# Optimization experiments

Measured on AMD Instinct MI355X. Metric: run time of the kernel, lower is better.

The kernel has to match this reference:

```python
import math
import jax, jax.numpy as jnp
import numpy as np

N, DIN, DOUT = 32768, 1024, 1024
C = 1.0            # ball curvature c (k = -c)
MIN_NORM = 1e-15
EPS_PROJ = 4e-3    # geoopt float32 boundary eps


def _safe_norm(x):
    # sqrt of clipped sum-of-squares: finite value and finite grad at 0
    return jnp.sqrt(jnp.clip(jnp.sum(x * x, axis=-1, keepdims=True), MIN_NORM))


def _artanh(u):
    return jnp.arctanh(jnp.clip(u, -1.0 + 1e-5, 1.0 - 1e-5))


def _project(x, c):
    norm = _safe_norm(x)
    maxnorm = (1.0 - EPS_PROJ) / jnp.sqrt(c)
    return jnp.where(norm > maxnorm, x / norm * maxnorm, x)


def _mobius_matvec(W, x, c):
    sqc = jnp.sqrt(c)
    x_norm = _safe_norm(x)                       # [N,1]
    mx = x @ W.T                                 # [N,DOUT]
    mx_norm = _safe_norm(mx)                     # [N,1]
    res = jnp.tanh(mx_norm / x_norm * _artanh(sqc * x_norm)) * mx / (mx_norm * sqc)
    zero = jnp.all(mx == 0, axis=-1, keepdims=True)
    return jnp.where(zero, jnp.zeros((), x.dtype), res)


def _expmap0(u, c):
    sqc = jnp.sqrt(c)
    u_norm = _safe_norm(u)
    return jnp.tanh(sqc * u_norm) * u / (sqc * u_norm)


def _mobius_add(x, y, c):
    x2 = jnp.sum(x * x, axis=-1, keepdims=True)
    y2 = jnp.sum(y * y, axis=-1, keepdims=True)
    xy = jnp.sum(x * y, axis=-1, keepdims=True)
    num = (1.0 + 2.0 * c * xy + c * y2) * x + (1.0 - c * x2) * y
    denom = 1.0 + 2.0 * c * xy + c * c * x2 * y2
    return num / jnp.clip(denom, MIN_NORM)


def setup_inputs() -> dict:
    key = jax.random.key(0)
    kx, kw, kb = jax.random.split(key, 3)
    x = jax.random.normal(kx, (N, DIN), jnp.float32)
    # place points strictly inside the unit Poincare ball
    x = x / (jnp.linalg.norm(x, axis=-1, keepdims=True) + 1.0) * 0.7
    limit = math.sqrt(2.0) * math.sqrt(6.0 / (DIN + DOUT))  # xavier_uniform gain=sqrt(2)
    weight = jax.random.uniform(kw, (DOUT, DIN), jnp.float32, -limit, limit)
    bias = 0.01 * jax.random.normal(kb, (DOUT,), jnp.float32)
    return {"x": x, "weight": weight, "bias": bias}


def reference(x, weight, bias) -> jnp.ndarray:
    c = jnp.float32(C)
    res = _mobius_matvec(weight, x, c)           # dropout=0 / eval: weight used as-is
    res = _project(res, c)
    hyp_bias = _project(_expmap0(bias[None, :], c), c)
    res = _project(_mobius_add(res, hyp_bias, c), c)
    return res
```

## Files before the change

kernel.cpp:

```cpp
#include <hip/hip_runtime.h>
#include <hip/hip_bf16.h>
#include <cmath>

#define NROWS 32768
#define DIN   1024
#define DOUT  1024
#define BM    64
#define BK    32
#define NKT   (DIN / BK)
#define MAXNORM 0.996f
#define XPAD  40

typedef __attribute__((ext_vector_type(8))) __bf16 bf16x8;
typedef __attribute__((ext_vector_type(4))) float  f32x4;
typedef __attribute__((ext_vector_type(2))) float  f32x2;
typedef __attribute__((ext_vector_type(4))) unsigned u32x4;

__device__ __forceinline__ unsigned pack2bf(float a, float b) {
    union { unsigned u; __bf16 h[2]; } p;
    p.h[0] = (__bf16)a; p.h[1] = (__bf16)b;
    return p.u;
}

__global__ void conv_w_kernel(const float* __restrict__ Wf, __bf16* __restrict__ Wb) {
    int c  = blockIdx.x * blockDim.x + threadIdx.x;
    int l  = c & 63;
    int j  = (c >> 6) & 63;
    int kt = c >> 12;
    int n  = j * 16 + (l & 15);
    int k0 = kt * 32 + (l >> 4) * 8;
    const float* src = Wf + (size_t)n * DIN + k0;
    f32x4 v0 = __builtin_nontemporal_load((const f32x4*)src);
    f32x4 v1 = __builtin_nontemporal_load((const f32x4*)(src + 4));
    u32x4 o;
    o.x = pack2bf(v0[0], v0[1]); o.y = pack2bf(v0[2], v0[3]);
    o.z = pack2bf(v1[0], v1[1]); o.w = pack2bf(v1[2], v1[3]);
    *(u32x4*)((char*)Wb + (size_t)c * 16) = o;
}

__global__ __launch_bounds__(1024) void hyp_kernel_reg(
    const float* __restrict__ X,
    const __bf16* __restrict__ Wb,
    const float* __restrict__ bias,
    float* __restrict__ out)
{
    __shared__ __align__(16) __bf16 Xt[4][BM * XPAD];
    __shared__ float hbs[DOUT];
    __shared__ float xsqs[BM];
    __shared__ float fco[BM][2];
    __shared__ float bred[16];

    const int tid  = threadIdx.x;
    const int lane = tid & 63;
    const int wid  = tid >> 6;
    const int l15  = lane & 15;
    const int l4   = lane >> 4;
    const int row0 = blockIdx.x * BM;

    const int xr = tid >> 4;
    const int xk = (tid & 15) * 2;
    const float* xp = X + (size_t)(row0 + xr) * DIN + xk;
    float xsq = 0.f;

    const __bf16* wp = Wb + ((size_t)(wid * 4) * 64 + lane) * 8;

    f32x4 acc[4][4];
    #pragma unroll
    for (int m = 0; m < 4; m++)
        #pragma unroll
        for (int n = 0; n < 4; n++)
            acc[m][n] = (f32x4){0.f, 0.f, 0.f, 0.f};

    f32x2 x0 = __builtin_nontemporal_load((const f32x2*)xp);
    f32x2 x1 = __builtin_nontemporal_load((const f32x2*)(xp + BK));
    bf16x8 bfr[4];
    #pragma unroll
    for (int i = 0; i < 4; i++) bfr[i] = *(const bf16x8*)(wp + i * 512);

    float bv = bias[tid];
    float bs = bv * bv;
    #pragma unroll
    for (int m = 1; m < 64; m <<= 1) bs += __shfl_xor(bs, m);
    if (lane == 0) bred[wid] = bs;
    __syncthreads();
    float tot = 0.f;
    #pragma unroll
    for (int i = 0; i < 16; i++) tot += bred[i];
    const float bnorm = sqrtf(fmaxf(tot, 1e-15f));
    const float bth   = tanhf(bnorm);
    float sc0 = bth / bnorm;
    float hn  = bth;
    if (hn > MAXNORM) { sc0 *= MAXNORM / hn; hn = MAXNORM; }
    hbs[tid] = sc0 * bv;
    const float y2c = hn * hn;

    xsq += x0[0] * x0[0] + x0[1] * x0[1];
    *(unsigned*)((char*)(&Xt[0][0]) + xr * (XPAD * 2) + xk * 2) = pack2bf(x0[0], x0[1]);
    x0 = x1;
    x1 = __builtin_nontemporal_load((const f32x2*)(xp + 2 * BK));

    auto step = [&](int s, int rb, int wb) {
        asm volatile("s_waitcnt lgkmcnt(0)" ::: "memory");
        __builtin_amdgcn_s_barrier();
        __builtin_amdgcn_sched_barrier(0);

        const char* xb = (const char*)(&Xt[rb][0]);
        bf16x8 a[4];
        #pragma unroll
        for (int m = 0; m < 4; m++)
            a[m] = *(const bf16x8*)(xb + ((m << 4) + l15) * (XPAD * 2) + (l4 << 4));

        if (s + 1 < NKT) {
            xsq += x0[0] * x0[0] + x0[1] * x0[1];
            *(unsigned*)((char*)(&Xt[wb][0]) + xr * (XPAD * 2) + xk * 2) = pack2bf(x0[0], x0[1]);
        }
        x0 = x1;
        int sf = s + 3 < NKT ? s + 3 : NKT - 1;
        x1 = __builtin_nontemporal_load((const f32x2*)(xp + (size_t)sf * BK));

        __builtin_amdgcn_s_setprio(1);
        #pragma unroll
        for (int n = 0; n < 4; n++)
            #pragma unroll
            for (int m = 0; m < 4; m++)
                acc[m][n] = __builtin_amdgcn_mfma_f32_16x16x32_bf16(a[m], bfr[n], acc[m][n], 0, 0, 0);
        __builtin_amdgcn_s_setprio(0);

        int sb = s + 1 < NKT ? s + 1 : NKT - 1;
        const __bf16* wkp = wp + (size_t)sb * 32768;
        #pragma unroll
        for (int i = 0; i < 4; i++) bfr[i] = *(const bf16x8*)(wkp + i * 512);
    };

    for (int s = 0; s < NKT; s += 4) {
        step(s + 0, 0, 1);
        step(s + 1, 1, 2);
        step(s + 2, 2, 3);
        step(s + 3, 3, 0);
    }

    __syncthreads();

    float* redq = (float*)(&Xt[0][0]);
    float* redd = redq + BM * 16;

    float xs = xsq;
    #pragma unroll
    for (int m = 1; m < 16; m <<= 1) xs += __shfl_xor(xs, m);
    if (l15 == 0) xsqs[xr] = xs;

    float hv[4];
    #pragma unroll
    for (int n = 0; n < 4; n++) hv[n] = hbs[(wid << 6) + (n << 4) + l15];

    #pragma unroll
    for (int m = 0; m < 4; m++) {
        #pragma unroll
        for (int r = 0; r < 4; r++) {
            float s = 0.f, d = 0.f;
            #pragma unroll
            for (int n = 0; n < 4; n++) {
                float v = acc[m][n][r];
                s += v * v;
                d += v * hv[n];
            }
            #pragma unroll
            for (int mm = 1; mm < 16; mm <<= 1) {
                s += __shfl_xor(s, mm);
                d += __shfl_xor(d, mm);
            }
            if (l15 == 0) {
                int rl = (m << 4) + (l4 << 2) + r;
                redq[rl * 16 + wid] = s;
                redd[rl * 16 + wid] = d;
            }
        }
    }
    __syncthreads();

    if (tid < BM) {
        int r = tid;
        float sq = 0.f, dt = 0.f;
        #pragma unroll
        for (int w = 0; w < 16; w++) { sq += redq[r * 16 + w]; dt += redd[r * 16 + w]; }
        float sx     = xsqs[r];
        float xnorm  = sqrtf(fmaxf(sx, 1e-15f));
        float mxnorm = sqrtf(fmaxf(sq, 1e-15f));
        float u  = fminf(xnorm, 1.f - 1e-5f);
        float tv = tanhf(mxnorm / xnorm * atanhf(u));
        float rn = fminf(tv, MAXNORM);
        float s  = rn / mxnorm;
        float xy = s * dt;
        float x2 = rn * rn;
        float Am = 1.f + 2.f * xy + y2c;
        float Bm = 1.f - x2;
        float Dm = fmaxf(1.f + 2.f * xy + x2 * y2c, 1e-15f);
        float g1 = Am * s / Dm;
        float g2 = Bm / Dm;
        float osq   = g1 * g1 * sq + 2.f * g1 * g2 * dt + g2 * g2 * y2c;
        float onorm = sqrtf(fmaxf(osq, 1e-15f));
        float psc   = onorm > MAXNORM ? MAXNORM / onorm : 1.f;
        fco[r][0] = g1 * psc;
        fco[r][1] = g2 * psc;
    }
    __syncthreads();

    #pragma unroll
    for (int m = 0; m < 4; m++) {
        #pragma unroll
        for (int r = 0; r < 4; r++) {
            int rl = (m << 4) + (l4 << 2) + r;
            float F1 = fco[rl][0], F2 = fco[rl][1];
            float* orow = out + (size_t)(row0 + rl) * DOUT + (wid << 6);
            #pragma unroll
            for (int n = 0; n < 4; n++)
                orow[(n << 4) + l15] = F1 * acc[m][n][r] + F2 * hv[n];
        }
    }
}

__global__ __launch_bounds__(512, 2) void hyp_kernel_basic(
    const float* __restrict__ X,
    const float* __restrict__ Wf,
    const float* __restrict__ bias,
    float* __restrict__ out)
{
    __shared__ __align__(16) __bf16 Wt[2][DOUT * BK];
    __shared__ __align__(16) __bf16 Xt[2][BM * XPAD];
    __shared__ float hbs[DOUT];
    __shared__ float redq[BM][8];
    __shared__ float redd[BM][8];
    __shared__ float xsqs[BM];
    __shared__ float fco[BM][2];
    __shared__ float bred[8];

    const int tid  = threadIdx.x;
    const int lane = tid & 63;
    const int wid  = tid >> 6;
    const int l15  = lane & 15;
    const int l4   = lane >> 4;
    const int row0 = blockIdx.x * BM;
    const int xr = tid >> 3;
    const int xk = (tid & 7) * 4;
    const float* xp = X + (size_t)(row0 + xr) * DIN + xk;
    float xsq = 0.f;

    f32x4 acc[4][8];
    #pragma unroll
    for (int m = 0; m < 4; m++)
        #pragma unroll
        for (int nt = 0; nt < 8; nt++)
            acc[m][nt] = (f32x4){0.f, 0.f, 0.f, 0.f};

    auto STAGE = [&](int buf, int kt) {
        if (kt < NKT) {
            #pragma unroll
            for (int j = 0; j < 8; j++) {
                int c = (j << 9) + tid;
                int q = c & 3, n = c >> 2;
                int k0 = kt * BK + ((q ^ ((n >> 1) & 3)) << 3);
                const float* src = Wf + (size_t)n * DIN + k0;
                f32x4 v0 = *(const f32x4*)src;
                f32x4 v1 = *(const f32x4*)(src + 4);
                u32x4 o;
                o.x = pack2bf(v0[0], v0[1]); o.y = pack2bf(v0[2], v0[3]);
                o.z = pack2bf(v1[0], v1[1]); o.w = pack2bf(v1[2], v1[3]);
                *(u32x4*)((char*)(&Wt[buf][0]) + c * 16) = o;
            }
            f32x4 xv = *(const f32x4*)(xp + kt * BK);
            xsq += xv[0]*xv[0] + xv[1]*xv[1] + xv[2]*xv[2] + xv[3]*xv[3];
            uint2 pk;
            pk.x = pack2bf(xv[0], xv[1]);
            pk.y = pack2bf(xv[2], xv[3]);
            *(uint2*)((char*)(&Xt[buf][0]) + xr * (XPAD * 2) + xk * 2) = pk;
        }
    };

    STAGE(0, 0);

    float b0 = bias[tid], b1 = bias[tid + 512];
    float bs = b0 * b0 + b1 * b1;
    #pragma unroll
    for (int m = 1; m < 64; m <<= 1) bs += __shfl_xor(bs, m);
    if (lane == 0) bred[wid] = bs;
    __syncthreads();
    float tot = 0.f;
    #pragma unroll
    for (int i = 0; i < 8; i++) tot += bred[i];
    const float bnorm = sqrtf(fmaxf(tot, 1e-15f));
    const float bth   = tanhf(bnorm);
    float sc0 = bth / bnorm;
    float hn  = bth;
    if (hn > MAXNORM) { sc0 *= MAXNORM / hn; hn = MAXNORM; }
    hbs[tid]       = sc0 * b0;
    hbs[tid + 512] = sc0 * b1;
    const float y2c = hn * hn;
    __syncthreads();

    float hv[8];
    #pragma unroll
    for (int nt = 0; nt < 8; nt++) hv[nt] = hbs[(wid << 7) + (nt << 4) + l15];

    int cur = 0;
    for (int kt = 0; kt < NKT; kt++) {
        STAGE(cur ^ 1, kt + 1);
        const char* xb = (const char*)(&Xt[cur][0]);
        const char* wb = (const char*)(&Wt[cur][0]);
        bf16x8 a[4], b[8];
        #pragma unroll
        for (int m = 0; m < 4; m++)
            a[m] = *(const bf16x8*)(xb + ((m << 4) + l15) * (XPAD * 2) + (l4 << 4));
        #pragma unroll
        for (int nt = 0; nt < 8; nt++) {
            int n = (wid << 7) + (nt << 4) + l15;
            b[nt] = *(const bf16x8*)(wb + n * 64 + ((l4 ^ ((n >> 1) & 3)) << 4));
        }
        #pragma unroll
        for (int m = 0; m < 4; m++)
            #pragma unroll
            for (int nt = 0; nt < 8; nt++)
                acc[m][nt] = __builtin_amdgcn_mfma_f32_16x16x32_bf16(a[m], b[nt], acc[m][nt], 0, 0, 0);
        __syncthreads();
        cur ^= 1;
    }

    float xs = xsq;
    #pragma unroll
    for (int m = 1; m < 8; m <<= 1) xs += __shfl_xor(xs, m);
    if ((tid & 7) == 0) xsqs[xr] = xs;

    #pragma unroll
    for (int m = 0; m < 4; m++) {
        #pragma unroll
        for (int r = 0; r < 4; r++) {
            float s = 0.f, d = 0.f;
            #pragma unroll
            for (int nt = 0; nt < 8; nt++) {
                float v = acc[m][nt][r];
                s += v * v;
                d += v * hv[nt];
            }
            #pragma unroll
            for (int mm = 1; mm < 16; mm <<= 1) {
                s += __shfl_xor(s, mm);
                d += __shfl_xor(d, mm);
            }
            if (l15 == 0) {
                int rl = (m << 4) + (l4 << 2) + r;
                redq[rl][wid] = s;
                redd[rl][wid] = d;
            }
        }
    }
    __syncthreads();

    if (tid < BM) {
        int r = tid;
        float sq = 0.f, dt = 0.f;
        #pragma unroll
        for (int w = 0; w < 8; w++) { sq += redq[r][w]; dt += redd[r][w]; }
        float sx     = xsqs[r];
        float xnorm  = sqrtf(fmaxf(sx, 1e-15f));
        float mxnorm = sqrtf(fmaxf(sq, 1e-15f));
        float u  = fminf(xnorm, 1.f - 1e-5f);
        float tv = tanhf(mxnorm / xnorm * atanhf(u));
        float rn = fminf(tv, MAXNORM);
        float s  = rn / mxnorm;
        float xy = s * dt;
        float x2 = rn * rn;
        float Am = 1.f + 2.f * xy + y2c;
        float Bm = 1.f - x2;
        float Dm = fmaxf(1.f + 2.f * xy + x2 * y2c, 1e-15f);
        float g1 = Am * s / Dm;
        float g2 = Bm / Dm;
        float osq   = g1 * g1 * sq + 2.f * g1 * g2 * dt + g2 * g2 * y2c;
        float onorm = sqrtf(fmaxf(osq, 1e-15f));
        float psc   = onorm > MAXNORM ? MAXNORM / onorm : 1.f;
        fco[r][0] = g1 * psc;
        fco[r][1] = g2 * psc;
    }
    __syncthreads();

    #pragma unroll
    for (int m = 0; m < 4; m++) {
        #pragma unroll
        for (int r = 0; r < 4; r++) {
            int rl = (m << 4) + (l4 << 2) + r;
            float F1 = fco[rl][0], F2 = fco[rl][1];
            float* orow = out + (size_t)(row0 + rl) * DOUT + (wid << 7);
            #pragma unroll
            for (int nt = 0; nt < 8; nt++)
                orow[(nt << 4) + l15] = F1 * acc[m][nt][r] + F2 * hv[nt];
        }
    }
}

extern "C" void kernel_launch(void* const* d_in, const int* in_sizes, int n_in,
                              void* d_out, int out_size, void* d_ws, size_t ws_size,
                              hipStream_t stream) {
    const float* X    = (const float*)d_in[0];
    const float* W    = (const float*)d_in[1];
    const float* bias = (const float*)d_in[2];
    float* out = (float*)d_out;

    const size_t wb_bytes = (size_t)DOUT * DIN * 2;
    if (ws_size >= wb_bytes) {
        __bf16* Wb = (__bf16*)d_ws;
        conv_w_kernel<<<dim3(512), dim3(256), 0, stream>>>(W, Wb);
        hyp_kernel_reg<<<dim3(NROWS / BM), dim3(1024), 0, stream>>>(X, Wb, bias, out);
    } else {
        hyp_kernel_basic<<<dim3(NROWS / BM), dim3(512), 0, stream>>>(X, W, bias, out);
    }
}
```

Baseline: 137.2 us.

## Shrink row tile to 32 with 512-thread blocks and wider per-wave column slabs

The register-resident weight kernel now uses 32-row tiles and 512 threads, with each wave owning 128 output columns (8 MFMA column tiles by 2 row tiles) instead of 64. The launch bounds ask for 4 blocks per CU, which gives more blocks and finer-grained scheduling. Each wave loads twice as many weight fragments per k-step, but each weight fragment is reused across fewer rows, so total weight traffic per output row goes up. The X staging store is moved ahead of the barrier, and nontemporal loads are replaced with ordinary loads.

```diff
diff --git a/kernel.cpp b/kernel.cpp
--- a/kernel.cpp
+++ b/kernel.cpp
@@ -5,7 +5,7 @@
 #define NROWS 32768
 #define DIN   1024
 #define DOUT  1024
-#define BM    64
+#define BM    32
 #define BK    32
 #define NKT   (DIN / BK)
 #define MAXNORM 0.996f
@@ -30,15 +30,15 @@
     int n  = j * 16 + (l & 15);
     int k0 = kt * 32 + (l >> 4) * 8;
     const float* src = Wf + (size_t)n * DIN + k0;
-    f32x4 v0 = __builtin_nontemporal_load((const f32x4*)src);
-    f32x4 v1 = __builtin_nontemporal_load((const f32x4*)(src + 4));
+    f32x4 v0 = *(const f32x4*)src;
+    f32x4 v1 = *(const f32x4*)(src + 4);
     u32x4 o;
     o.x = pack2bf(v0[0], v0[1]); o.y = pack2bf(v0[2], v0[3]);
     o.z = pack2bf(v1[0], v1[1]); o.w = pack2bf(v1[2], v1[3]);
     *(u32x4*)((char*)Wb + (size_t)c * 16) = o;
 }
 
-__global__ __launch_bounds__(1024) void hyp_kernel_reg(
+__global__ __launch_bounds__(512, 4) void hyp_kernel_reg(
     const float* __restrict__ X,
     const __bf16* __restrict__ Wb,
     const float* __restrict__ bias,
@@ -48,7 +48,7 @@
     __shared__ float hbs[DOUT];
     __shared__ float xsqs[BM];
     __shared__ float fco[BM][2];
-    __shared__ float bred[16];
+    __shared__ float bred[8];
 
     const int tid  = threadIdx.x;
     const int lane = tid & 63;
@@ -62,74 +62,75 @@
     const float* xp = X + (size_t)(row0 + xr) * DIN + xk;
     float xsq = 0.f;
 
-    const __bf16* wp = Wb + ((size_t)(wid * 4) * 64 + lane) * 8;
-
-    f32x4 acc[4][4];
-    #pragma unroll
-    for (int m = 0; m < 4; m++)
-        #pragma unroll
-        for (int n = 0; n < 4; n++)
+    const __bf16* wp = Wb + ((size_t)(wid * 8) * 64 + lane) * 8;
+
+    f32x4 acc[2][8];
+    #pragma unroll
+    for (int m = 0; m < 2; m++)
+        #pragma unroll
+        for (int n = 0; n < 8; n++)
             acc[m][n] = (f32x4){0.f, 0.f, 0.f, 0.f};
 
-    f32x2 x0 = __builtin_nontemporal_load((const f32x2*)xp);
-    f32x2 x1 = __builtin_nontemporal_load((const f32x2*)(xp + BK));
-    bf16x8 bfr[4];
-    #pragma unroll
-    for (int i = 0; i < 4; i++) bfr[i] = *(const bf16x8*)(wp + i * 512);
-
-    float bv = bias[tid];
-    float bs = bv * bv;
+    f32x2 x0 = *(const f32x2*)xp;
+    f32x2 x1 = *(const f32x2*)(xp + BK);
+    bf16x8 bfr[8];
+    #pragma unroll
+    for (int i = 0; i < 8; i++) bfr[i] = *(const bf16x8*)(wp + i * 512);
+
+    float b0 = bias[tid], b1 = bias[tid + 512];
+    float bs = b0 * b0 + b1 * b1;
     #pragma unroll
     for (int m = 1; m < 64; m <<= 1) bs += __shfl_xor(bs, m);
     if (lane == 0) bred[wid] = bs;
     __syncthreads();
     float tot = 0.f;
     #pragma unroll
-    for (int i = 0; i < 16; i++) tot += bred[i];
+    for (int i = 0; i < 8; i++) tot += bred[i];
     const float bnorm = sqrtf(fmaxf(tot, 1e-15f));
     const float bth   = tanhf(bnorm);
     float sc0 = bth / bnorm;
     float hn  = bth;
     if (hn > MAXNORM) { sc0 *= MAXNORM / hn; hn = MAXNORM; }
-    hbs[tid] = sc0 * bv;
+    hbs[tid]       = sc0 * b0;
+    hbs[tid + 512] = sc0 * b1;
     const float y2c = hn * hn;
 
     xsq += x0[0] * x0[0] + x0[1] * x0[1];
     *(unsigned*)((char*)(&Xt[0][0]) + xr * (XPAD * 2) + xk * 2) = pack2bf(x0[0], x0[1]);
     x0 = x1;
-    x1 = __builtin_nontemporal_load((const f32x2*)(xp + 2 * BK));
+    x1 = *(const f32x2*)(xp + 2 * BK);
 
     auto step = [&](int s, int rb, int wb) {
+        if (s + 1 < NKT) {
+            xsq += x0[0] * x0[0] + x0[1] * x0[1];
+            *(unsigned*)((char*)(&Xt[wb][0]) + xr * (XPAD * 2) + xk * 2) = pack2bf(x0[0], x0[1]);
+        }
+        x0 = x1;
+        int sf = s + 3 < NKT ? s + 3 : NKT - 1;
+        x1 = *(const f32x2*)(xp + (size_t)sf * BK);
+
         asm volatile("s_waitcnt lgkmcnt(0)" ::: "memory");
         __builtin_amdgcn_s_barrier();
         __builtin_amdgcn_sched_barrier(0);
 
         const char* xb = (const char*)(&Xt[rb][0]);
-        bf16x8 a[4];
-        #pragma unroll
-        for (int m = 0; m < 4; m++)
+        bf16x8 a[2];
+        #pragma unroll
+        for (int m = 0; m < 2; m++)
             a[m] = *(const bf16x8*)(xb + ((m << 4) + l15) * (XPAD * 2) + (l4 << 4));
 
-        if (s + 1 < NKT) {
-            xsq += x0[0] * x0[0] + x0[1] * x0[1];
-            *(unsigned*)((char*)(&Xt[wb][0]) + xr * (XPAD * 2) + xk * 2) = pack2bf(x0[0], x0[1]);
-        }
-        x0 = x1;
-        int sf = s + 3 < NKT ? s + 3 : NKT - 1;
-        x1 = __builtin_nontemporal_load((const f32x2*)(xp + (size_t)sf * BK));
-
         __builtin_amdgcn_s_setprio(1);
         #pragma unroll
-        for (int n = 0; n < 4; n++)
-            #pragma unroll
-            for (int m = 0; m < 4; m++)
+        for (int n = 0; n < 8; n++)
+            #pragma unroll
+            for (int m = 0; m < 2; m++)
                 acc[m][n] = __builtin_amdgcn_mfma_f32_16x16x32_bf16(a[m], bfr[n], acc[m][n], 0, 0, 0);
         __builtin_amdgcn_s_setprio(0);
 
         int sb = s + 1 < NKT ? s + 1 : NKT - 1;
         const __bf16* wkp = wp + (size_t)sb * 32768;
         #pragma unroll
-        for (int i = 0; i < 4; i++) bfr[i] = *(const bf16x8*)(wkp + i * 512);
+        for (int i = 0; i < 8; i++) bfr[i] = *(const bf16x8*)(wkp + i * 512);
     };
 
     for (int s = 0; s < NKT; s += 4) {
@@ -142,24 +143,24 @@
     __syncthreads();
 
     float* redq = (float*)(&Xt[0][0]);
-    float* redd = redq + BM * 16;
+    float* redd = redq + BM * 8;
 
     float xs = xsq;
     #pragma unroll
     for (int m = 1; m < 16; m <<= 1) xs += __shfl_xor(xs, m);
     if (l15 == 0) xsqs[xr] = xs;
 
-    float hv[4];
-    #pragma unroll
-    for (int n = 0; n < 4; n++) hv[n] = hbs[(wid << 6) + (n << 4) + l15];
-
-    #pragma unroll
-    for (int m = 0; m < 4; m++) {
+    float hv[8];
+    #pragma unroll
+    for (int n = 0; n < 8; n++) hv[n] = hbs[(wid << 7) + (n << 4) + l15];
+
+    #pragma unroll
+    for (int m = 0; m < 2; m++) {
         #pragma unroll
         for (int r = 0; r < 4; r++) {
             float s = 0.f, d = 0.f;
             #pragma unroll
-            for (int n = 0; n < 4; n++) {
+            for (int n = 0; n < 8; n++) {
                 float v = acc[m][n][r];
                 s += v * v;
                 d += v * hv[n];
@@ -171,8 +172,8 @@
             }
             if (l15 == 0) {
                 int rl = (m << 4) + (l4 << 2) + r;
-                redq[rl * 16 + wid] = s;
-                redd[rl * 16 + wid] = d;
+                redq[rl * 8 + wid] = s;
+                redd[rl * 8 + wid] = d;
             }
         }
     }
@@ -182,7 +183,7 @@
         int r = tid;
         float sq = 0.f, dt = 0.f;
         #pragma unroll
-        for (int w = 0; w < 16; w++) { sq += redq[r * 16 + w]; dt += redd[r * 16 + w]; }
+        for (int w = 0; w < 8; w++) { sq += redq[r * 8 + w]; dt += redd[r * 8 + w]; }
         float sx     = xsqs[r];
         float xnorm  = sqrtf(fmaxf(sx, 1e-15f));
         float mxnorm = sqrtf(fmaxf(sq, 1e-15f));
@@ -206,14 +207,14 @@
     __syncthreads();
 
     #pragma unroll
-    for (int m = 0; m < 4; m++) {
+    for (int m = 0; m < 2; m++) {
         #pragma unroll
         for (int r = 0; r < 4; r++) {
             int rl = (m << 4) + (l4 << 2) + r;
             float F1 = fco[rl][0], F2 = fco[rl][1];
-            float* orow = out + (size_t)(row0 + rl) * DOUT + (wid << 6);
-            #pragma unroll
-            for (int n = 0; n < 4; n++)
+            float* orow = out + (size_t)(row0 + rl) * DOUT + (wid << 7);
+            #pragma unroll
+            for (int n = 0; n < 8; n++)
                 orow[(n << 4) + l15] = F1 * acc[m][n][r] + F2 * hv[n];
         }
     }
@@ -226,12 +227,12 @@
     float* __restrict__ out)
 {
     __shared__ __align__(16) __bf16 Wt[2][DOUT * BK];
-    __shared__ __align__(16) __bf16 Xt[2][BM * XPAD];
+    __shared__ __align__(16) __bf16 Xt[2][64 * XPAD];
     __shared__ float hbs[DOUT];
-    __shared__ float redq[BM][8];
-    __shared__ float redd[BM][8];
-    __shared__ float xsqs[BM];
-    __shared__ float fco[BM][2];
+    __shared__ float redq[64][8];
+    __shared__ float redd[64][8];
+    __shared__ float xsqs[64];
+    __shared__ float fco[64][2];
     __shared__ float bred[8];
 
     const int tid  = threadIdx.x;
@@ -239,7 +240,7 @@
     const int wid  = tid >> 6;
     const int l15  = lane & 15;
     const int l4   = lane >> 4;
-    const int row0 = blockIdx.x * BM;
+    const int row0 = blockIdx.x * 64;
     const int xr = tid >> 3;
     const int xk = (tid & 7) * 4;
     const float* xp = X + (size_t)(row0 + xr) * DIN + xk;
@@ -354,7 +355,7 @@
     }
     __syncthreads();
 
-    if (tid < BM) {
+    if (tid < 64) {
         int r = tid;
         float sq = 0.f, dt = 0.f;
         #pragma unroll
@@ -407,8 +408,8 @@
     if (ws_size >= wb_bytes) {
         __bf16* Wb = (__bf16*)d_ws;
         conv_w_kernel<<<dim3(512), dim3(256), 0, stream>>>(W, Wb);
-        hyp_kernel_reg<<<dim3(NROWS / BM), dim3(1024), 0, stream>>>(X, Wb, bias, out);
+        hyp_kernel_reg<<<dim3(NROWS / BM), dim3(512), 0, stream>>>(X, Wb, bias, out);
     } else {
-        hyp_kernel_basic<<<dim3(NROWS / BM), dim3(512), 0, stream>>>(X, W, bias, out);
+        hyp_kernel_basic<<<dim3(NROWS / 64), dim3(512), 0, stream>>>(X, W, bias, out);
     }
 }
```

Result: slower. 191.4 us (+39.4%).

## Stage full X tile in XOR-swizzled LDS with chunked loads and fewer barriers

Applied to the files above, without the earlier changes.

The 1024-thread main kernel no longer keeps a 4-deep ring of small per-K-step X buffers. It now stores the whole 64x1024 bf16 X tile in shared memory (128 KB) with an XOR swizzle. X is loaded and stored in chunks of four K-steps, so the kernel has one barrier per chunk instead of one per K-step, and the loads switch from nontemporal to plain. This is meant to cut barrier and synchronisation overhead and bank conflicts, at the cost of much larger LDS use and less fine-grained overlap between global loads and MFMA.

```diff
diff --git a/kernel.cpp b/kernel.cpp
--- a/kernel.cpp
+++ b/kernel.cpp
@@ -30,21 +30,21 @@
     int n  = j * 16 + (l & 15);
     int k0 = kt * 32 + (l >> 4) * 8;
     const float* src = Wf + (size_t)n * DIN + k0;
-    f32x4 v0 = __builtin_nontemporal_load((const f32x4*)src);
-    f32x4 v1 = __builtin_nontemporal_load((const f32x4*)(src + 4));
+    f32x4 v0 = *(const f32x4*)src;
+    f32x4 v1 = *(const f32x4*)(src + 4);
     u32x4 o;
     o.x = pack2bf(v0[0], v0[1]); o.y = pack2bf(v0[2], v0[3]);
     o.z = pack2bf(v1[0], v1[1]); o.w = pack2bf(v1[2], v1[3]);
     *(u32x4*)((char*)Wb + (size_t)c * 16) = o;
 }
 
-__global__ __launch_bounds__(1024) void hyp_kernel_reg(
+__global__ __launch_bounds__(1024) void hyp_kernel_xp(
     const float* __restrict__ X,
     const __bf16* __restrict__ Wb,
     const float* __restrict__ bias,
     float* __restrict__ out)
 {
-    __shared__ __align__(16) __bf16 Xt[4][BM * XPAD];
+    __shared__ __align__(16) __bf16 Xl[BM * DIN];
     __shared__ float hbs[DOUT];
     __shared__ float xsqs[BM];
     __shared__ float fco[BM][2];
@@ -57,9 +57,11 @@
     const int l4   = lane >> 4;
     const int row0 = blockIdx.x * BM;
 
-    const int xr = tid >> 4;
-    const int xk = (tid & 15) * 2;
-    const float* xp = X + (size_t)(row0 + xr) * DIN + xk;
+    const int xr  = tid >> 4;
+    const int xi  = tid & 15;
+    const float* xp = X + (size_t)(row0 + xr) * DIN + xi * 2;
+    const int xmask = (xr & 15) << 4;
+    char* xlrow = (char*)Xl + xr * 2048;
     float xsq = 0.f;
 
     const __bf16* wp = Wb + ((size_t)(wid * 4) * 64 + lane) * 8;
@@ -71,8 +73,22 @@
         for (int n = 0; n < 4; n++)
             acc[m][n] = (f32x4){0.f, 0.f, 0.f, 0.f};
 
-    f32x2 x0 = __builtin_nontemporal_load((const f32x2*)xp);
-    f32x2 x1 = __builtin_nontemporal_load((const f32x2*)(xp + BK));
+    f32x2 xq[4];
+    auto xload = [&](int c) {
+        #pragma unroll
+        for (int j = 0; j < 4; j++)
+            xq[j] = *(const f32x2*)(xp + (size_t)(c * 4 + j) * BK);
+    };
+    auto xstore = [&](int c) {
+        #pragma unroll
+        for (int j = 0; j < 4; j++) {
+            xsq += xq[j][0] * xq[j][0] + xq[j][1] * xq[j][1];
+            int kb = (c * 4 + j) * 64 + xi * 4;
+            *(unsigned*)(xlrow + (kb ^ xmask)) = pack2bf(xq[j][0], xq[j][1]);
+        }
+    };
+
+    xload(0);
     bf16x8 bfr[4];
     #pragma unroll
     for (int i = 0; i < 4; i++) bfr[i] = *(const bf16x8*)(wp + i * 512);
@@ -94,54 +110,44 @@
     hbs[tid] = sc0 * bv;
     const float y2c = hn * hn;
 
-    xsq += x0[0] * x0[0] + x0[1] * x0[1];
-    *(unsigned*)((char*)(&Xt[0][0]) + xr * (XPAD * 2) + xk * 2) = pack2bf(x0[0], x0[1]);
-    x0 = x1;
-    x1 = __builtin_nontemporal_load((const f32x2*)(xp + 2 * BK));
-
-    auto step = [&](int s, int rb, int wb) {
-        asm volatile("s_waitcnt lgkmcnt(0)" ::: "memory");
-        __builtin_amdgcn_s_barrier();
-        __builtin_amdgcn_sched_barrier(0);
-
-        const char* xb = (const char*)(&Xt[rb][0]);
-        bf16x8 a[4];
-        #pragma unroll
-        for (int m = 0; m < 4; m++)
-            a[m] = *(const bf16x8*)(xb + ((m << 4) + l15) * (XPAD * 2) + (l4 << 4));
-
-        if (s + 1 < NKT) {
-            xsq += x0[0] * x0[0] + x0[1] * x0[1];
-            *(unsigned*)((char*)(&Xt[wb][0]) + xr * (XPAD * 2) + xk * 2) = pack2bf(x0[0], x0[1]);
-        }
-        x0 = x1;
-        int sf = s + 3 < NKT ? s + 3 : NKT - 1;
-        x1 = __builtin_nontemporal_load((const f32x2*)(xp + (size_t)sf * BK));
-
-        __builtin_amdgcn_s_setprio(1);
-        #pragma unroll
-        for (int n = 0; n < 4; n++)
-            #pragma unroll
-            for (int m = 0; m < 4; m++)
-                acc[m][n] = __builtin_amdgcn_mfma_f32_16x16x32_bf16(a[m], bfr[n], acc[m][n], 0, 0, 0);
-        __builtin_amdgcn_s_setprio(0);
-
-        int sb = s + 1 < NKT ? s + 1 : NKT - 1;
-        const __bf16* wkp = wp + (size_t)sb * 32768;
-        #pragma unroll
-        for (int i = 0; i < 4; i++) bfr[i] = *(const bf16x8*)(wkp + i * 512);
-    };
-
-    for (int s = 0; s < NKT; s += 4) {
-        step(s + 0, 0, 1);
-        step(s + 1, 1, 2);
-        step(s + 2, 2, 3);
-        step(s + 3, 3, 0);
-    }
-
-    __syncthreads();
-
-    float* redq = (float*)(&Xt[0][0]);
+    xstore(0);
+    xload(1);
+    asm volatile("s_waitcnt lgkmcnt(0)" ::: "memory");
+    __builtin_amdgcn_s_barrier();
+    __builtin_amdgcn_sched_barrier(0);
+
+    #pragma unroll
+    for (int c = 0; c < 8; c++) {
+        #pragma unroll
+        for (int j = 0; j < 4; j++) {
+            const int kt = c * 4 + j;
+            __builtin_amdgcn_s_setprio(1);
+            #pragma unroll
+            for (int m = 0; m < 4; m++) {
+                bf16x8 a = *(const bf16x8*)((char*)Xl + (m * 16 + l15) * 2048 +
+                             ((kt * 64 + (l4 << 4)) ^ (l15 << 4)));
+                #pragma unroll
+                for (int n = 0; n < 4; n++)
+                    acc[m][n] = __builtin_amdgcn_mfma_f32_16x16x32_bf16(a, bfr[n], acc[m][n], 0, 0, 0);
+            }
+            __builtin_amdgcn_s_setprio(0);
+            const int sb = (kt + 1 < NKT) ? kt + 1 : NKT - 1;
+            const __bf16* wkp = wp + (size_t)sb * 32768;
+            #pragma unroll
+            for (int i = 0; i < 4; i++) bfr[i] = *(const bf16x8*)(wkp + i * 512);
+        }
+        if (c < 7) {
+            xstore(c + 1);
+            if (c < 6) xload(c + 2);
+            asm volatile("s_waitcnt lgkmcnt(0)" ::: "memory");
+            __builtin_amdgcn_s_barrier();
+            __builtin_amdgcn_sched_barrier(0);
+        }
+    }
+
+    __syncthreads();
+
+    float* redq = (float*)(&Xl[0]);
     float* redd = redq + BM * 16;
 
     float xs = xsq;
@@ -226,12 +232,12 @@
     float* __restrict__ out)
 {
     __shared__ __align__(16) __bf16 Wt[2][DOUT * BK];
-    __shared__ __align__(16) __bf16 Xt[2][BM * XPAD];
+    __shared__ __align__(16) __bf16 Xt[2][64 * XPAD];
     __shared__ float hbs[DOUT];
-    __shared__ float redq[BM][8];
-    __shared__ float redd[BM][8];
-    __shared__ float xsqs[BM];
-    __shared__ float fco[BM][2];
+    __shared__ float redq[64][8];
+    __shared__ float redd[64][8];
+    __shared__ float xsqs[64];
+    __shared__ float fco[64][2];
     __shared__ float bred[8];
 
     const int tid  = threadIdx.x;
@@ -239,7 +245,7 @@
     const int wid  = tid >> 6;
     const int l15  = lane & 15;
     const int l4   = lane >> 4;
-    const int row0 = blockIdx.x * BM;
+    const int row0 = blockIdx.x * 64;
     const int xr = tid >> 3;
     const int xk = (tid & 7) * 4;
     const float* xp = X + (size_t)(row0 + xr) * DIN + xk;
@@ -354,7 +360,7 @@
     }
     __syncthreads();
 
-    if (tid < BM) {
+    if (tid < 64) {
         int r = tid;
         float sq = 0.f, dt = 0.f;
         #pragma unroll
@@ -407,8 +413,8 @@
     if (ws_size >= wb_bytes) {
         __bf16* Wb = (__bf16*)d_ws;
         conv_w_kernel<<<dim3(512), dim3(256), 0, stream>>>(W, Wb);
-        hyp_kernel_reg<<<dim3(NROWS / BM), dim3(1024), 0, stream>>>(X, Wb, bias, out);
+        hyp_kernel_xp<<<dim3(NROWS / BM), dim3(1024), 0, stream>>>(X, Wb, bias, out);
     } else {
-        hyp_kernel_basic<<<dim3(NROWS / BM), dim3(512), 0, stream>>>(X, W, bias, out);
+        hyp_kernel_basic<<<dim3(NROWS / 64), dim3(512), 0, stream>>>(X, W, bias, out);
     }
 }
```

Measured after the change: 161.2 us. 1.17x slower.
